# Kernel optimization log

Measured on AMD Instinct MI355X. Metric: run time of the kernel, lower is better.

The kernel has to match this reference:

```python
import jax, jax.numpy as jnp
import numpy as np

H, W, C = 384, 384, 200
HIDE, CNN_OUT, NCLS = 128, 64, 16
N = H * W
E = 1179648
EPS = 1e-5  # torch BatchNorm eps


def _bn(x, g, b, axes):
    # training-mode batch norm (biased variance), matches torch BN in train mode
    m = x.mean(axes, keepdims=True)
    v = x.var(axes, keepdims=True)
    return (x - m) * jax.lax.rsqrt(v + EPS) * g + b


def _gcn(x, w, bias, src, dst, n):
    # PyG GCNConv: add self loops, symmetric D^-1/2 (A+I) D^-1/2 normalization
    h = x @ w  # [N, out]
    loop = jnp.arange(n, dtype=src.dtype)
    s = jnp.concatenate([src, loop])
    d = jnp.concatenate([dst, loop])
    deg = jax.ops.segment_sum(jnp.ones(s.shape, x.dtype), d, num_segments=n)
    dinv = jnp.where(deg > 0, jax.lax.rsqrt(jnp.maximum(deg, 1.0)) * (deg > 0), 0.0)
    norm = dinv[s] * dinv[d]  # [E+N]
    out = jax.ops.segment_sum(h[s] * norm[:, None], d, num_segments=n)
    return out + bias


def _gnn_layer(x, bn_g, bn_b, w, b, src, dst):
    # F.normalize (row L2) -> BN1d -> GCNConv -> LeakyReLU (dropout off in eval)
    nrm = jnp.linalg.norm(x, axis=1, keepdims=True)
    x = x / jnp.maximum(nrm, 1e-12)
    x = _bn(x, bn_g, bn_b, (0,))
    return jax.nn.leaky_relu(_gcn(x, w, b, src, dst, x.shape[0]))


def setup_inputs() -> dict:
    key = jax.random.key(0)
    ks = jax.random.split(key, 16)
    p = {}
    p["x"] = jax.random.normal(ks[0], (H, W, C), jnp.float32)
    p["edge_index"] = jax.random.randint(ks[1], (2, E), 0, N, jnp.int32)
    # CNN_denoise: BN(C) -> 1x1 conv C->128 -> BN(128) -> 1x1 conv 128->128
    p["dn_bn1_g"] = jnp.ones((C,), jnp.float32); p["dn_bn1_b"] = jnp.zeros((C,), jnp.float32)
    p["dn_w1"] = jax.random.normal(ks[2], (C, HIDE), jnp.float32) * 0.05
    p["dn_b1"] = jnp.zeros((HIDE,), jnp.float32)
    p["dn_bn2_g"] = jnp.ones((HIDE,), jnp.float32); p["dn_bn2_b"] = jnp.zeros((HIDE,), jnp.float32)
    p["dn_w2"] = jax.random.normal(ks[3], (HIDE, HIDE), jnp.float32) * 0.05
    p["dn_b2"] = jnp.zeros((HIDE,), jnp.float32)
    # CNNCONV(128,64,k=5): BN(128) -> point 1x1 128->64 (no bias) -> depthwise 5x5 (bias)
    p["cnn_bn_g"] = jnp.ones((HIDE,), jnp.float32); p["cnn_bn_b"] = jnp.zeros((HIDE,), jnp.float32)
    p["cnn_pw"] = jax.random.normal(ks[4], (HIDE, CNN_OUT), jnp.float32) * 0.05
    p["cnn_dw"] = jax.random.normal(ks[5], (CNN_OUT, 1, 5, 5), jnp.float32) * 0.05
    p["cnn_db"] = jnp.zeros((CNN_OUT,), jnp.float32)
    # GCN branch: GNN(128,128), GNN(128,128), GNN(128,64)
    dims = [(HIDE, HIDE), (HIDE, HIDE), (HIDE, CNN_OUT)]
    for i, (di, do) in enumerate(dims, 1):
        p[f"g{i}_bn_g"] = jnp.ones((di,), jnp.float32)
        p[f"g{i}_bn_b"] = jnp.zeros((di,), jnp.float32)
        p[f"g{i}_w"] = jax.random.normal(ks[5 + i], (di, do), jnp.float32) * 0.05
        p[f"g{i}_b"] = jnp.zeros((do,), jnp.float32)
    p["lin_w"] = jax.random.normal(ks[9], (HIDE, NCLS), jnp.float32) * 0.05
    p["lin_b"] = jnp.zeros((NCLS,), jnp.float32)
    return p


def reference(x, edge_index,
              dn_bn1_g, dn_bn1_b, dn_w1, dn_b1, dn_bn2_g, dn_bn2_b, dn_w2, dn_b2,
              cnn_bn_g, cnn_bn_b, cnn_pw, cnn_dw, cnn_db,
              g1_bn_g, g1_bn_b, g1_w, g1_b,
              g2_bn_g, g2_bn_b, g2_w, g2_b,
              g3_bn_g, g3_bn_b, g3_w, g3_b,
              lin_w, lin_b):
    src, dst = edge_index[0], edge_index[1]
    # CNN_denoise (channel-last; 1x1 convs are matmuls)
    h = _bn(x, dn_bn1_g, dn_bn1_b, (0, 1))
    h = jax.nn.leaky_relu(h @ dn_w1 + dn_b1)
    h = _bn(h, dn_bn2_g, dn_bn2_b, (0, 1))
    clean = jax.nn.leaky_relu(h @ dn_w2 + dn_b2)       # [H,W,128]
    flat = clean.reshape(N, HIDE)
    # CNN branch: BN -> 1x1 -> LeakyReLU -> depthwise 5x5 -> LeakyReLU
    c = _bn(clean, cnn_bn_g, cnn_bn_b, (0, 1))
    c = jax.nn.leaky_relu(c @ cnn_pw)                  # [H,W,64]
    cn = c.transpose(2, 0, 1)[None]                    # [1,64,H,W]
    cn = jax.lax.conv_general_dilated(
        cn, cnn_dw, (1, 1), 'SAME', feature_group_count=CNN_OUT,
        dimension_numbers=('NCHW', 'OIHW', 'NCHW'))
    cn = jax.nn.leaky_relu(cn[0].transpose(1, 2, 0) + cnn_db)
    cnn_res = cn.reshape(N, CNN_OUT)
    # GCN branch (3 layers)
    g = _gnn_layer(flat, g1_bn_g, g1_bn_b, g1_w, g1_b, src, dst)
    g = _gnn_layer(g, g2_bn_g, g2_bn_b, g2_w, g2_b, src, dst)
    g = _gnn_layer(g, g3_bn_g, g3_bn_b, g3_w, g3_b, src, dst)
    y = jnp.concatenate([g, cnn_res], axis=-1) @ lin_w + lin_b
    return jax.nn.softmax(y, axis=-1)
```

## Files before the change

### kernel.cpp

```cpp
#include <hip/hip_runtime.h>
#include <stddef.h>

#define HH 384
#define WW 384
#define CC 200
#define NN 147456
#define EE 1179648
#define HIDE 128
#define COUT 64
#define NCLS 16
#define BN_EPS 1e-5f

#define SREP 16
#define SLOTF (512 * SREP)

using u16 = unsigned short;
typedef __attribute__((ext_vector_type(8))) short short8;
typedef __attribute__((ext_vector_type(4))) float float4v;

__device__ __forceinline__ float b2f(u16 u) {
    union { unsigned int i; float f; } v; v.i = ((unsigned int)u) << 16; return v.f;
}
__device__ __forceinline__ u16 f2b(float f) {
    union { float f; unsigned int i; } v; v.f = f;
    unsigned int x = v.i;
    unsigned int r = (x + 0x7fffu + ((x >> 16) & 1u)) >> 16;
    return (u16)r;
}
__device__ __forceinline__ float lrelu(float v) { return v > 0.f ? v : 0.01f * v; }

__global__ void sniff(const u16* __restrict__ x, int* __restrict__ flag) {
    __shared__ int cntS;
    if (threadIdx.x == 0) cntS = 0;
    __syncthreads();
    int c = 0;
    for (int i = 0; i < 8; i++) {
        u16 h = x[threadIdx.x * 8 + i];
        int hb = (h >> 8) & 0x7F;
        if (hb >= 0x3C && hb <= 0x41) c++;
    }
    atomicAdd(&cntS, c);
    __syncthreads();
    if (threadIdx.x == 0) *flag = (cntS < 1536) ? 1 : 0;
}

#define NPAR 27
struct PConv { const void* src[NPAR]; int n[NPAR]; int off[NPAR]; };

__global__ void convert_params(PConv pc, const int* __restrict__ flag,
                               u16* __restrict__ dst) {
    int b = blockIdx.x;
    int n = pc.n[b];
    const void* s = pc.src[b];
    u16* d = dst + pc.off[b];
    int isf = *flag;
    if (isf) {
        const float* sf = (const float*)s;
        for (int i = threadIdx.x; i < n; i += 256) d[i] = f2b(sf[i]);
    } else {
        const u16* sh = (const u16*)s;
        for (int i = threadIdx.x; i < n; i += 256) d[i] = sh[i];
    }
}

__global__ __launch_bounds__(256) void stats200(const void* __restrict__ X,
                                                const int* __restrict__ flag,
                                                float* __restrict__ arena) {
    __shared__ __align__(16) u16 s[128 * 200];
    int t = threadIdx.x;
    int r0 = blockIdx.x * 128;
    if (*flag) {
        const float* Xf = (const float*)X;
        for (int i = t; i < 128 * 25; i += 256) {
            int r = i / 25, kc = i - r * 25;
            const float* p = Xf + (size_t)(r0 + r) * CC + kc * 8;
            float4v a = *(const float4v*)p;
            float4v b = *(const float4v*)(p + 4);
            short8 v;
            #pragma unroll
            for (int j = 0; j < 4; j++) { v[j] = (short)f2b(a[j]); v[4 + j] = (short)f2b(b[j]); }
            *(short8*)&s[r * 200 + kc * 8] = v;
        }
    } else {
        const u16* Xh = (const u16*)X;
        for (int i = t; i < 128 * 25; i += 256) {
            int r = i / 25, kc = i - r * 25;
            *(short8*)&s[r * 200 + kc * 8] =
                *(const short8*)(Xh + (size_t)(r0 + r) * CC + kc * 8);
        }
    }
    __syncthreads();
    if (t < CC) {
        float sum = 0.f, sq = 0.f;
        for (int r = 0; r < 128; r++) {
            float v = b2f(s[r * 200 + t]);
            sum += v; sq += v * v;
        }
        float* rep = arena + (blockIdx.x & (SREP - 1)) * 512;
        atomicAdd(&rep[t], sum);
        atomicAdd(&rep[256 + t], sq);
    }
}

template<int K, int KPAD, int O>
__global__ __launch_bounds__(256) void fold_bn(
        const float* __restrict__ arena, float invN,
        const u16* __restrict__ bng, const u16* __restrict__ bnb,
        const u16* __restrict__ Wsrc, const u16* __restrict__ extrab,
        u16* __restrict__ WT, float* __restrict__ cb) {
    __shared__ float aS[KPAD], sS[KPAD];
    int t = threadIdx.x;
    if (t < KPAD) {
        float a = 0.f, sh = 0.f;
        if (t < K) {
            float sum = 0.f, sq = 0.f;
            #pragma unroll
            for (int r = 0; r < SREP; r++) {
                sum += arena[r * 512 + t];
                sq  += arena[r * 512 + 256 + t];
            }
            float m = sum * invN;
            float var = fmaxf(sq * invN - m * m, 0.f);
            a = b2f(bng[t]) * rsqrtf(var + BN_EPS);
            sh = b2f(bnb[t]) - m * a;
        }
        aS[t] = a; sS[t] = sh;
    }
    __syncthreads();
    int g = t >> 6, l = t & 63;
    int o = blockIdx.x * 4 + g;
    if (o < O) {
        float c = 0.f;
        #pragma unroll
        for (int k = l; k < KPAD; k += 64) {
            float w = (k < K) ? b2f(Wsrc[k * O + o]) : 0.f;
            c += sS[k] * w;
            WT[o * KPAD + k] = f2b(aS[k] * w);
        }
        #pragma unroll
        for (int s = 32; s >= 1; s >>= 1) c += __shfl_down(c, s);
        if (l == 0) cb[o] = c + (extrab ? b2f(extrab[o]) : 0.f);
    }
}

template<int KT, int KSRC, int O, bool LEAKY, bool SCALE, int STATS, bool DUAL>
__global__ __launch_bounds__(256) void gemm_mfma(
        const void* __restrict__ Ap, const u16* __restrict__ WT,
        const float* __restrict__ cb, const float* __restrict__ s1,
        const float* __restrict__ s2, const int* __restrict__ f32p,
        u16* __restrict__ out, float* __restrict__ stA,
        float* __restrict__ stB, float* __restrict__ invn,
        u16* __restrict__ out2) {
    constexpr int KPAD = KT * 32;
    constexpr int LDA = KPAD + 8;
    constexpr int CHR = KPAD / 8;
    constexpr int CHD = KSRC / 8;
    constexpr int NCT = O / 16;
    constexpr int CPW = NCT / 4;
    __shared__ __align__(16) u16 As[64 * LDA];
    __shared__ float rS[4][64];
    __shared__ float invS[64];
    __shared__ float sS1[64], sS2[64];
    int tid = threadIdx.x;
    int row0 = blockIdx.x * 64;

    int isf = f32p ? *f32p : 0;
    if (isf) {
        const float* A = (const float*)Ap;
        for (int i = tid; i < 64 * CHR; i += 256) {
            int r = i / CHR, kc = i - r * CHR;
            short8 v = {0, 0, 0, 0, 0, 0, 0, 0};
            if (kc < CHD) {
                const float* p = A + (size_t)(row0 + r) * KSRC + kc * 8;
                float4v a = *(const float4v*)p;
                float4v b = *(const float4v*)(p + 4);
                #pragma unroll
                for (int j = 0; j < 4; j++) { v[j] = (short)f2b(a[j]); v[4 + j] = (short)f2b(b[j]); }
            }
            *(short8*)&As[r * LDA + kc * 8] = v;
        }
    } else {
        const u16* A = (const u16*)Ap;
        for (int i = tid; i < 64 * CHR; i += 256) {
            int r = i / CHR, kc = i - r * CHR;
            short8 v = {0, 0, 0, 0, 0, 0, 0, 0};
            if (kc < CHD)
                v = *(const short8*)(A + (size_t)(row0 + r) * KSRC + kc * 8);
            *(short8*)&As[r * LDA + kc * 8] = v;
        }
    }
    if (SCALE && tid < 64) { sS1[tid] = s1[row0 + tid]; sS2[tid] = s2[row0 + tid]; }
    __syncthreads();

    int w = tid >> 6, lane = tid & 63, m = lane & 15, q = lane >> 4;
    float4v acc[4][CPW];
    #pragma unroll
    for (int mf = 0; mf < 4; mf++)
        #pragma unroll
        for (int cp = 0; cp < CPW; cp++)
            acc[mf][cp] = (float4v){0.f, 0.f, 0.f, 0.f};

    const u16* Abp = &As[m * LDA + q * 8];
    const u16* Bbp = WT + (size_t)((w * CPW) * 16 + m) * KPAD + q * 8;

    #pragma unroll
    for (int kt = 0; kt < KT; kt++) {
        short8 af[4];
        #pragma unroll
        for (int mf = 0; mf < 4; mf++)
            af[mf] = *(const short8*)(Abp + mf * 16 * LDA + kt * 32);
        #pragma unroll
        for (int cp = 0; cp < CPW; cp++) {
            short8 bf = *(const short8*)(Bbp + (size_t)cp * 16 * KPAD + kt * 32);
            #pragma unroll
            for (int mf = 0; mf < 4; mf++)
                acc[mf][cp] = __builtin_amdgcn_mfma_f32_16x16x32_bf16(
                    af[mf], bf, acc[mf][cp], 0, 0, 0);
        }
    }

    float rp[4][4] = {};
    #pragma unroll
    for (int cp = 0; cp < CPW; cp++) {
        int ct = w * CPW + cp;
        int col = ct * 16 + m;
        float cbv = cb[col];
        #pragma unroll
        for (int mf = 0; mf < 4; mf++) {
            #pragma unroll
            for (int r = 0; r < 4; r++) {
                int rl = mf * 16 + q * 4 + r;
                float x = acc[mf][cp][r];
                if constexpr (DUAL) {
                    if (ct < 8) {
                        x = (x * sS1[rl] + cbv) * sS2[rl];
                        out[(size_t)(row0 + rl) * 128 + col] = f2b(x);
                    } else {
                        x = lrelu(x + cbv);
                        out2[(size_t)(row0 + rl) * 64 + (col - 128)] = f2b(x);
                    }
                } else {
                    if constexpr (SCALE) x = (x * sS1[rl] + cbv) * sS2[rl];
                    else                 x += cbv;
                    if constexpr (LEAKY) x = lrelu(x);
                    out[(size_t)(row0 + rl) * O + col] = f2b(x);
                }
                acc[mf][cp][r] = x;
                if constexpr (STATS == 2) rp[mf][r] += x * x;
            }
        }
    }

    if constexpr (STATS == 2) {
        #pragma unroll
        for (int mf = 0; mf < 4; mf++) {
            #pragma unroll
            for (int r = 0; r < 4; r++) {
                float v = rp[mf][r];
                v += __shfl_xor(v, 1); v += __shfl_xor(v, 2);
                v += __shfl_xor(v, 4); v += __shfl_xor(v, 8);
                if (m == 0) rS[w][mf * 16 + q * 4 + r] = v;
            }
        }
        __syncthreads();
        if (tid < 64) {
            float ss = rS[0][tid] + rS[1][tid] + rS[2][tid] + rS[3][tid];
            float inv = 1.0f / fmaxf(sqrtf(ss), 1e-12f);
            invS[tid] = inv;
            invn[row0 + tid] = inv;
        }
        __syncthreads();
    }

    if constexpr (STATS >= 1) {
        float* stAr = stA + (blockIdx.x & (SREP - 1)) * 512;
        float* stBr = (STATS == 2) ? stB + (blockIdx.x & (SREP - 1)) * 512 : nullptr;
        #pragma unroll
        for (int cp = 0; cp < CPW; cp++) {
            int col = (w * CPW + cp) * 16 + m;
            float cs = 0.f, cq = 0.f, ns = 0.f, nq = 0.f;
            #pragma unroll
            for (int mf = 0; mf < 4; mf++) {
                #pragma unroll
                for (int r = 0; r < 4; r++) {
                    float x = acc[mf][cp][r];
                    cs += x; cq += x * x;
                    if constexpr (STATS == 2) {
                        float nv = x * invS[mf * 16 + q * 4 + r];
                        ns += nv; nq += nv * nv;
                    }
                }
            }
            cs += __shfl_xor(cs, 16); cs += __shfl_xor(cs, 32);
            cq += __shfl_xor(cq, 16); cq += __shfl_xor(cq, 32);
            if constexpr (STATS == 2) {
                ns += __shfl_xor(ns, 16); ns += __shfl_xor(ns, 32);
                nq += __shfl_xor(nq, 16); nq += __shfl_xor(nq, 32);
            }
            if (q == 0) {
                atomicAdd(&stAr[col], cs);
                atomicAdd(&stAr[256 + col], cq);
                if constexpr (STATS == 2) {
                    atomicAdd(&stBr[col], ns);
                    atomicAdd(&stBr[256 + col], nq);
                }
            }
        }
    }
}

__global__ void hist(const int* __restrict__ dst, int* __restrict__ cnt) {
    int e = blockIdx.x * 256 + threadIdx.x;
    unsigned d = (unsigned)dst[e];
    if (d < (unsigned)NN) atomicAdd(&cnt[d], 1);
}
__global__ void mkdinv(const int* __restrict__ cnt, float* __restrict__ dinv) {
    int i = blockIdx.x * 256 + threadIdx.x;
    int c = cnt[i]; if (c < 0) c = 0;
    dinv[i] = rsqrtf((float)c + 1.0f);
}
__global__ void scan_part(const int* __restrict__ cnt, int* __restrict__ bsum) {
    int b = blockIdx.x, t = threadIdx.x;
    int base = b * 1024 + t * 4;
    int s = cnt[base] + cnt[base + 1] + cnt[base + 2] + cnt[base + 3];
    #pragma unroll
    for (int o = 32; o >= 1; o >>= 1) s += __shfl_down(s, o);
    __shared__ int ws4[4];
    if ((t & 63) == 0) ws4[t >> 6] = s;
    __syncthreads();
    if (t == 0) bsum[b] = ws4[0] + ws4[1] + ws4[2] + ws4[3];
}
__global__ void scan_top(const int* __restrict__ bsum, int* __restrict__ boff) {
    if (threadIdx.x == 0) {
        int a = 0;
        for (int i = 0; i < 144; i++) { boff[i] = a; a += bsum[i]; }
    }
}
__global__ void scan_write(const int* __restrict__ cnt, const int* __restrict__ boff,
                           int* __restrict__ offv) {
    int b = blockIdx.x, t = threadIdx.x;
    int base = b * 1024 + t * 4;
    int v0 = cnt[base], v1 = cnt[base + 1], v2 = cnt[base + 2], v3 = cnt[base + 3];
    int ts = v0 + v1 + v2 + v3;
    __shared__ int sc[256];
    sc[t] = ts;
    __syncthreads();
    for (int o = 1; o < 256; o <<= 1) {
        int x = (t >= o) ? sc[t - o] : 0;
        __syncthreads();
        sc[t] += x;
        __syncthreads();
    }
    int excl = boff[b] + sc[t] - ts;
    offv[base] = excl;
    offv[base + 1] = excl + v0;
    offv[base + 2] = excl + v0 + v1;
    offv[base + 3] = excl + v0 + v1 + v2;
    if (b == 143 && t == 255) offv[NN] = excl + ts;
}
__global__ void scatter(const int* __restrict__ src, const int* __restrict__ dst,
                        int* __restrict__ cursor, const int* __restrict__ offv,
                        int* __restrict__ csr) {
    int e = blockIdx.x * 256 + threadIdx.x;
    unsigned d = (unsigned)dst[e];
    if (d >= (unsigned)NN) return;
    int p = atomicAdd(&cursor[d], 1);
    unsigned idx = (unsigned)(offv[d] + p);
    if (idx < (unsigned)EE) csr[idx] = src[e];
}

template<int O, int STATS, int GRP>
__global__ __launch_bounds__(256) void aggregate(
        const u16* __restrict__ h2, const int* __restrict__ offv,
        const int* __restrict__ csr, const float* __restrict__ dinv,
        const u16* __restrict__ gb, u16* __restrict__ outp,
        float* __restrict__ stA, float* __restrict__ invn) {
    constexpr int CH = O / 8;
    constexpr int NPB = 256 / CH;
    __shared__ float colS[O], colQ[O];
    int t = threadIdx.x;
    if (STATS && t < O) { colS[t] = 0.f; colQ[t] = 0.f; }
    int local = t / CH, c = t % CH;
    size_t cof = (size_t)c * 8;
    const u16* hb = h2 + cof;
    short8 gv = *(const short8*)(gb + cof);
    float sreg[8] = {0.f, 0.f, 0.f, 0.f, 0.f, 0.f, 0.f, 0.f};
    float qreg[8] = {0.f, 0.f, 0.f, 0.f, 0.f, 0.f, 0.f, 0.f};

    #pragma unroll
    for (int g = 0; g < GRP; g++) {
        int d = blockIdx.x * (NPB * GRP) + g * NPB + local;
        float acc[8];
        short8 selfv = *(const short8*)(hb + (size_t)d * O);
        #pragma unroll
        for (int j = 0; j < 8; j++) acc[j] = b2f((u16)selfv[j]);
        int e0 = offv[d], e1 = offv[d + 1];
        if (e0 < 0) e0 = 0;
        if (e1 > EE) e1 = EE;
        int k = e0;
        int nq = (e1 - e0) >> 2;
        unsigned ia = 0, ib = 0, ic2 = 0, id2 = 0;
        if (nq > 0) {
            ia  = (unsigned)csr[k];     ib  = (unsigned)csr[k + 1];
            ic2 = (unsigned)csr[k + 2]; id2 = (unsigned)csr[k + 3];
        }
        for (int qi = 0; qi < nq; qi++) {
            short8 va = *(const short8*)(hb + (size_t)ia * O);
            short8 vb = *(const short8*)(hb + (size_t)ib * O);
            short8 vc = *(const short8*)(hb + (size_t)ic2 * O);
            short8 vd = *(const short8*)(hb + (size_t)id2 * O);
            k += 4;
            if (qi + 1 < nq) {
                ia  = (unsigned)csr[k];     ib  = (unsigned)csr[k + 1];
                ic2 = (unsigned)csr[k + 2]; id2 = (unsigned)csr[k + 3];
            }
            #pragma unroll
            for (int j = 0; j < 8; j++)
                acc[j] += (b2f((u16)va[j]) + b2f((u16)vb[j])) +
                          (b2f((u16)vc[j]) + b2f((u16)vd[j]));
        }
        for (; k < e1; k++) {
            unsigned s = (unsigned)csr[k];
            short8 va = *(const short8*)(hb + (size_t)s * O);
            #pragma unroll
            for (int j = 0; j < 8; j++) acc[j] += b2f((u16)va[j]);
        }
        float dd = dinv[d];
        float outv[8];
        short8 res;
        #pragma unroll
        for (int j = 0; j < 8; j++) {
            outv[j] = lrelu(dd * acc[j] + b2f((u16)gv[j]));
            res[j] = (short)f2b(outv[j]);
        }
        *(short8*)(outp + (size_t)d * O + cof) = res;

        if constexpr (STATS) {
            float ss = 0.f;
            #pragma unroll
            for (int j = 0; j < 8; j++) ss += outv[j] * outv[j];
            ss += __shfl_xor(ss, 1); ss += __shfl_xor(ss, 2);
            ss += __shfl_xor(ss, 4); ss += __shfl_xor(ss, 8);
            float inv = 1.0f / fmaxf(sqrtf(ss), 1e-12f);
            if (c == 0) invn[d] = inv;
            #pragma unroll
            for (int j = 0; j < 8; j++) {
                float nv = outv[j] * inv;
                sreg[j] += nv; qreg[j] += nv * nv;
            }
        }
    }

    if constexpr (STATS) {
        __syncthreads();
        #pragma unroll
        for (int j = 0; j < 8; j++) {
            float s = sreg[j];
            s += __shfl_xor(s, 16); s += __shfl_xor(s, 32);
            float qq = qreg[j];
            qq += __shfl_xor(qq, 16); qq += __shfl_xor(qq, 32);
            if ((t & 63) < 16) {
                atomicAdd(&colS[c * 8 + j], s);
                atomicAdd(&colQ[c * 8 + j], qq);
            }
        }
        __syncthreads();
        if (t < O) {
            float* rep = stA + (blockIdx.x & (SREP - 1)) * 512;
            atomicAdd(&rep[t], colS[t]);
            atomicAdd(&rep[256 + t], colQ[t]);
        }
    }
}

__global__ __launch_bounds__(256) void final_fused(
        const u16* __restrict__ g3, const u16* __restrict__ cpre,
        const u16* __restrict__ dwW, const u16* __restrict__ db,
        const u16* __restrict__ lw, const u16* __restrict__ lb,
        const int* __restrict__ flag, void* __restrict__ outp) {
    __shared__ __align__(16) u16 tile[400 * 72];
    __shared__ __align__(16) u16 wT[25 * 64];
    __shared__ __align__(16) u16 wL[2048];
    __shared__ float bDW[64];
    __shared__ float bL[16];
    int t = threadIdx.x;
    int tx = blockIdx.x % 24, ty = blockIdx.x / 24;
    int x0 = tx * 16 - 2, y0 = ty * 16 - 2;
    for (int i = t; i < 1600; i += 256) {
        int f = i / 25, tap = i - f * 25;
        wT[tap * 64 + f] = dwW[i];
    }
    for (int i = t; i < 2048; i += 256) wL[i] = lw[i];
    if (t < 64) bDW[t] = b2f(db[t]);
    if (t < 16) bL[t] = b2f(lb[t]);
    for (int u = t; u < 3200; u += 256) {
        int pix = u >> 3, c8 = u & 7;
        int gy = y0 + pix / 20, gx = x0 + pix % 20;
        short8 v = {0, 0, 0, 0, 0, 0, 0, 0};
        if (gy >= 0 && gy < HH && gx >= 0 && gx < WW)
            v = *(const short8*)(cpre + ((size_t)(gy * WW + gx)) * 64 + c8 * 8);
        *(short8*)&tile[pix * 72 + c8 * 8] = v;
    }
    __syncthreads();

    int px = t & 15, py = t >> 4;
    int node = (ty * 16 + py) * WW + tx * 16 + px;
    float y[16];
    #pragma unroll
    for (int o = 0; o < 16; o++) y[o] = bL[o];

    const u16* g3p = g3 + (size_t)node * 64;
    for (int c8 = 0; c8 < 8; c8++) {
        short8 gvv = *(const short8*)(g3p + c8 * 8);
        #pragma unroll
        for (int j = 0; j < 8; j++) {
            float g = b2f((u16)gvv[j]);
            const short8 w0 = *(const short8*)&wL[(c8 * 8 + j) * 16];
            const short8 w1 = *(const short8*)&wL[(c8 * 8 + j) * 16 + 8];
            #pragma unroll
            for (int o = 0; o < 8; o++) {
                y[o]     += g * b2f((u16)w0[o]);
                y[o + 8] += g * b2f((u16)w1[o]);
            }
        }
    }
    for (int c8 = 0; c8 < 8; c8++) {
        float acc[8] = {0.f, 0.f, 0.f, 0.f, 0.f, 0.f, 0.f, 0.f};
        #pragma unroll
        for (int dy = 0; dy < 5; dy++) {
            int rbase = ((py + dy) * 20 + px) * 72 + c8 * 8;
            #pragma unroll
            for (int dx = 0; dx < 5; dx++) {
                short8 v  = *(const short8*)&tile[rbase + dx * 72];
                short8 wv = *(const short8*)&wT[(dy * 5 + dx) * 64 + c8 * 8];
                #pragma unroll
                for (int j = 0; j < 8; j++)
                    acc[j] += b2f((u16)v[j]) * b2f((u16)wv[j]);
            }
        }
        #pragma unroll
        for (int j = 0; j < 8; j++) {
            float cv = lrelu(acc[j] + bDW[c8 * 8 + j]);
            int f = 64 + c8 * 8 + j;
            const short8 w0 = *(const short8*)&wL[f * 16];
            const short8 w1 = *(const short8*)&wL[f * 16 + 8];
            #pragma unroll
            for (int o = 0; o < 8; o++) {
                y[o]     += cv * b2f((u16)w0[o]);
                y[o + 8] += cv * b2f((u16)w1[o]);
            }
        }
    }
    float mx = y[0];
    #pragma unroll
    for (int o = 1; o < 16; o++) mx = fmaxf(mx, y[o]);
    float sum = 0.f;
    #pragma unroll
    for (int o = 0; o < 16; o++) { y[o] = __expf(y[o] - mx); sum += y[o]; }
    float inv = 1.0f / fmaxf(sum, 1e-30f);
    if (*flag) {
        float* of = (float*)outp;
        #pragma unroll
        for (int o = 0; o < 16; o++) of[(size_t)node * 16 + o] = y[o] * inv;
    } else {
        u16* oh = (u16*)outp;
        #pragma unroll
        for (int o = 0; o < 16; o++) oh[(size_t)node * 16 + o] = f2b(y[o] * inv);
    }
}

extern "C" void kernel_launch(void* const* d_in, const int* in_sizes, int n_in,
                              void* d_out, int out_size, void* d_ws, size_t ws_size,
                              hipStream_t stream) {
    const void* X   = d_in[0];
    const int* EIDX = (const int*)d_in[1];
    const int* esrc = EIDX;
    const int* edst = EIDX + EE;

    char* ws = (char*)d_ws;
    size_t off = 0;
    auto alloc = [&](size_t sz) -> char* {
        size_t szr = (sz + 255) & ~(size_t)255;
        char* p;
        if (off + szr <= ws_size) { p = ws + off; off += szr; }
        else { p = ws; }
        return p;
    };

    int*   dflag   = (int*)alloc(256);
    static const int pidx[NPAR] = {2,3,4,5,6,7,8,9,10,11,12,13,14,
                                   15,16,17,18,19,20,21,22,23,24,25,26,27,28};
    static const int pn[NPAR]   = {200,200,25600,128,128,128,16384,128,
                                   128,128,8192,1600,64,
                                   128,128,16384,128,
                                   128,128,16384,128,
                                   128,128,8192,64,
                                   2048,16};
    u16* parena = (u16*)alloc(100352 * 2);
    PConv pc;
    {
        int po = 0;
        for (int i = 0; i < NPAR; i++) {
            pc.src[i] = d_in[pidx[i]];
            pc.n[i] = pn[i];
            pc.off[i] = po;
            po += (pn[i] + 15) & ~15;
        }
    }
    const u16* DN1G = parena + pc.off[0];
    const u16* DN1B = parena + pc.off[1];
    const u16* DNW1 = parena + pc.off[2];
    const u16* DNB1 = parena + pc.off[3];
    const u16* DN2G = parena + pc.off[4];
    const u16* DN2B = parena + pc.off[5];
    const u16* DNW2 = parena + pc.off[6];
    const u16* DNB2 = parena + pc.off[7];
    const u16* CBNG = parena + pc.off[8];
    const u16* CBNB = parena + pc.off[9];
    const u16* CPW  = parena + pc.off[10];
    const u16* CDW  = parena + pc.off[11];
    const u16* CDB  = parena + pc.off[12];
    const u16* G1G  = parena + pc.off[13];
    const u16* G1B  = parena + pc.off[14];
    const u16* G1W  = parena + pc.off[15];
    const u16* G1BI = parena + pc.off[16];
    const u16* G2G  = parena + pc.off[17];
    const u16* G2B  = parena + pc.off[18];
    const u16* G2W  = parena + pc.off[19];
    const u16* G2BI = parena + pc.off[20];
    const u16* G3G  = parena + pc.off[21];
    const u16* G3B  = parena + pc.off[22];
    const u16* G3W  = parena + pc.off[23];
    const u16* G3BI = parena + pc.off[24];
    const u16* LINW = parena + pc.off[25];
    const u16* LINB = parena + pc.off[26];

    int*   cnt     = (int*)alloc((size_t)NN * 4);
    int*   cursor  = (int*)alloc((size_t)NN * 4);
    float* arena   = (float*)alloc((size_t)6 * SLOTF * 4);
    int*   offv    = (int*)alloc((size_t)(NN + 1) * 4);
    int*   bsum    = (int*)alloc(144 * 4);
    int*   boff    = (int*)alloc(144 * 4);
    float* dinvp   = (float*)alloc((size_t)NN * 4);
    float* invnorm = (float*)alloc((size_t)NN * 4);
    u16*   W1T     = (u16*)alloc(128 * 224 * 2);
    u16*   W2T     = (u16*)alloc(128 * 128 * 2);
    u16*   WgT     = (u16*)alloc(192 * 128 * 2);
    float* cb1     = (float*)alloc(128 * 4);
    float* cb2     = (float*)alloc(128 * 4);
    float* cbg     = (float*)alloc(192 * 4);
    int*   csr     = (int*)alloc((size_t)EE * 4);
    u16*   cbuf    = (u16*)alloc((size_t)NN * 64 * 2);
    u16*   big1    = (u16*)alloc((size_t)NN * 128 * 2);
    u16*   big2    = (u16*)alloc((size_t)NN * 128 * 2);

    const float invN = 1.0f / (float)NN;
    size_t zsz = (size_t)((char*)(arena + 6 * SLOTF) - (char*)cnt);
    size_t zcap = ((char*)cnt >= ws && (size_t)((char*)cnt - ws) < ws_size)
                      ? ws_size - (size_t)((char*)cnt - ws) : 0;
    if (zsz > zcap) zsz = zcap;
    hipMemsetAsync(cnt, 0, zsz, stream);

    sniff<<<1, 256, 0, stream>>>((const u16*)X, dflag);
    convert_params<<<NPAR, 256, 0, stream>>>(pc, dflag, parena);

    hist<<<EE / 256, 256, 0, stream>>>(edst, cnt);
    mkdinv<<<NN / 256, 256, 0, stream>>>(cnt, dinvp);
    scan_part<<<144, 256, 0, stream>>>(cnt, bsum);
    scan_top<<<1, 64, 0, stream>>>(bsum, boff);
    scan_write<<<144, 256, 0, stream>>>(cnt, boff, offv);
    scatter<<<EE / 256, 256, 0, stream>>>(esrc, edst, cursor, offv, csr);

    stats200<<<1152, 256, 0, stream>>>(X, dflag, arena + 0 * SLOTF);
    fold_bn<200, 224, 128><<<32, 256, 0, stream>>>(arena + 0 * SLOTF, invN, DN1G, DN1B, DNW1, DNB1, W1T, cb1);
    gemm_mfma<7, 200, 128, true, false, 1, false><<<NN / 64, 256, 0, stream>>>(
        X, W1T, cb1, nullptr, nullptr, dflag, big1, arena + 1 * SLOTF, nullptr, nullptr, nullptr);
    fold_bn<128, 128, 128><<<32, 256, 0, stream>>>(arena + 1 * SLOTF, invN, DN2G, DN2B, DNW2, DNB2, W2T, cb2);
    gemm_mfma<4, 128, 128, true, false, 2, false><<<NN / 64, 256, 0, stream>>>(
        big1, W2T, cb2, nullptr, nullptr, nullptr, big2, arena + 2 * SLOTF, arena + 3 * SLOTF, invnorm, nullptr);

    fold_bn<128, 128, 128><<<32, 256, 0, stream>>>(arena + 3 * SLOTF, invN, G1G, G1B, G1W, nullptr, WgT, cbg);
    fold_bn<128, 128, 64><<<16, 256, 0, stream>>>(arena + 2 * SLOTF, invN, CBNG, CBNB, CPW, nullptr,
                                                  WgT + 128 * 128, cbg + 128);
    gemm_mfma<4, 128, 192, false, true, 0, true><<<NN / 64, 256, 0, stream>>>(
        big2, WgT, cbg, invnorm, dinvp, nullptr, big1, nullptr, nullptr, nullptr, cbuf);
    aggregate<128, 1, 4><<<NN / 64, 256, 0, stream>>>(
        big1, offv, csr, dinvp, G1BI, big2, arena + 4 * SLOTF, invnorm);

    fold_bn<128, 128, 128><<<32, 256, 0, stream>>>(arena + 4 * SLOTF, invN, G2G, G2B, G2W, nullptr, WgT, cbg);
    gemm_mfma<4, 128, 128, false, true, 0, false><<<NN / 64, 256, 0, stream>>>(
        big2, WgT, cbg, invnorm, dinvp, nullptr, big1, nullptr, nullptr, nullptr, nullptr);
    aggregate<128, 1, 4><<<NN / 64, 256, 0, stream>>>(
        big1, offv, csr, dinvp, G2BI, big2, arena + 5 * SLOTF, invnorm);

    fold_bn<128, 128, 64><<<16, 256, 0, stream>>>(arena + 5 * SLOTF, invN, G3G, G3B, G3W, nullptr, WgT, cbg);
    gemm_mfma<4, 128, 64, false, true, 0, false><<<NN / 64, 256, 0, stream>>>(
        big2, WgT, cbg, invnorm, dinvp, nullptr, big1, nullptr, nullptr, nullptr, nullptr);
    aggregate<64, 0, 1><<<NN / 32, 256, 0, stream>>>(
        big1, offv, csr, dinvp, G3BI, big2, nullptr, nullptr);

    final_fused<<<576, 256, 0, stream>>>(big2, cbuf, CDW, CDB, LINW, LINB, dflag, d_out);

    (void)in_sizes; (void)n_in; (void)out_size;
}
```

Before: 770.0 us.

## Sort nodes by degree for load-balanced GCN aggregation and unroll gather by 8

Builds a degree-bucketed permutation of nodes (histogram, scan, scatter) and makes each aggregate kernel process nodes in that order, so lanes in a wavefront handle similar-degree nodes and divergence drops. The neighbor gather loop is also restructured to issue 8 independent row loads per iteration with 4/2/1 tails, raising memory-level parallelism. The cost is three extra small kernels, an extra indirection through perm, and loss of spatial locality in output writes and self-row reads.

```diff
diff --git a/kernel.cpp b/kernel.cpp
--- a/kernel.cpp
+++ b/kernel.cpp
@@ -13,6 +13,7 @@
 
 #define SREP 16
 #define SLOTF (512 * SREP)
+#define DBINS 64
 
 using u16 = unsigned short;
 typedef __attribute__((ext_vector_type(8))) short short8;
@@ -369,12 +370,46 @@
     if (idx < (unsigned)EE) csr[idx] = src[e];
 }
 
+__global__ void deg_hist(const int* __restrict__ cnt, int* __restrict__ dbin) {
+    __shared__ int h[DBINS];
+    int t = threadIdx.x;
+    if (t < DBINS) h[t] = 0;
+    __syncthreads();
+    int i = blockIdx.x * 256 + t;
+    int dg = cnt[i]; if (dg < 0) dg = 0; if (dg > DBINS - 1) dg = DBINS - 1;
+    atomicAdd(&h[dg], 1);
+    __syncthreads();
+    if (t < DBINS) atomicAdd(&dbin[t], h[t]);
+}
+__global__ void deg_scan(const int* __restrict__ dbin, int* __restrict__ dbase) {
+    if (threadIdx.x == 0) {
+        int a = 0;
+        for (int b = DBINS - 1; b >= 0; b--) { dbase[b] = a; a += dbin[b]; }
+    }
+}
+__global__ void deg_scatter(const int* __restrict__ cnt, int* __restrict__ dbase,
+                            int* __restrict__ perm) {
+    __shared__ int h[DBINS], base[DBINS];
+    int t = threadIdx.x;
+    if (t < DBINS) h[t] = 0;
+    __syncthreads();
+    int i = blockIdx.x * 256 + t;
+    int dg = cnt[i]; if (dg < 0) dg = 0; if (dg > DBINS - 1) dg = DBINS - 1;
+    atomicAdd(&h[dg], 1);
+    __syncthreads();
+    if (t < DBINS) { base[t] = atomicAdd(&dbase[t], h[t]); h[t] = 0; }
+    __syncthreads();
+    int lp = atomicAdd(&h[dg], 1);
+    perm[base[dg] + lp] = i;
+}
+
 template<int O, int STATS, int GRP>
 __global__ __launch_bounds__(256) void aggregate(
         const u16* __restrict__ h2, const int* __restrict__ offv,
         const int* __restrict__ csr, const float* __restrict__ dinv,
         const u16* __restrict__ gb, u16* __restrict__ outp,
-        float* __restrict__ stA, float* __restrict__ invn) {
+        float* __restrict__ stA, float* __restrict__ invn,
+        const int* __restrict__ perm) {
     constexpr int CH = O / 8;
     constexpr int NPB = 256 / CH;
     __shared__ float colS[O], colQ[O];
@@ -389,7 +424,8 @@
 
     #pragma unroll
     for (int g = 0; g < GRP; g++) {
-        int d = blockIdx.x * (NPB * GRP) + g * NPB + local;
+        int pos = blockIdx.x * (NPB * GRP) + g * NPB + local;
+        int d = perm[pos];
         float acc[8];
         short8 selfv = *(const short8*)(hb + (size_t)d * O);
         #pragma unroll
@@ -398,32 +434,53 @@
         if (e0 < 0) e0 = 0;
         if (e1 > EE) e1 = EE;
         int k = e0;
-        int nq = (e1 - e0) >> 2;
-        unsigned ia = 0, ib = 0, ic2 = 0, id2 = 0;
-        if (nq > 0) {
-            ia  = (unsigned)csr[k];     ib  = (unsigned)csr[k + 1];
-            ic2 = (unsigned)csr[k + 2]; id2 = (unsigned)csr[k + 3];
-        }
-        for (int qi = 0; qi < nq; qi++) {
-            short8 va = *(const short8*)(hb + (size_t)ia * O);
-            short8 vb = *(const short8*)(hb + (size_t)ib * O);
-            short8 vc = *(const short8*)(hb + (size_t)ic2 * O);
-            short8 vd = *(const short8*)(hb + (size_t)id2 * O);
+        for (; k + 8 <= e1; k += 8) {
+            unsigned i0 = (unsigned)csr[k],     i1 = (unsigned)csr[k + 1];
+            unsigned i2 = (unsigned)csr[k + 2], i3 = (unsigned)csr[k + 3];
+            unsigned i4 = (unsigned)csr[k + 4], i5 = (unsigned)csr[k + 5];
+            unsigned i6 = (unsigned)csr[k + 6], i7 = (unsigned)csr[k + 7];
+            short8 v0 = *(const short8*)(hb + (size_t)i0 * O);
+            short8 v1 = *(const short8*)(hb + (size_t)i1 * O);
+            short8 v2 = *(const short8*)(hb + (size_t)i2 * O);
+            short8 v3 = *(const short8*)(hb + (size_t)i3 * O);
+            short8 v4 = *(const short8*)(hb + (size_t)i4 * O);
+            short8 v5 = *(const short8*)(hb + (size_t)i5 * O);
+            short8 v6 = *(const short8*)(hb + (size_t)i6 * O);
+            short8 v7 = *(const short8*)(hb + (size_t)i7 * O);
+            #pragma unroll
+            for (int j = 0; j < 8; j++)
+                acc[j] += ((b2f((u16)v0[j]) + b2f((u16)v1[j])) +
+                           (b2f((u16)v2[j]) + b2f((u16)v3[j]))) +
+                          ((b2f((u16)v4[j]) + b2f((u16)v5[j])) +
+                           (b2f((u16)v6[j]) + b2f((u16)v7[j])));
+        }
+        if (k + 4 <= e1) {
+            unsigned i0 = (unsigned)csr[k],     i1 = (unsigned)csr[k + 1];
+            unsigned i2 = (unsigned)csr[k + 2], i3 = (unsigned)csr[k + 3];
+            short8 v0 = *(const short8*)(hb + (size_t)i0 * O);
+            short8 v1 = *(const short8*)(hb + (size_t)i1 * O);
+            short8 v2 = *(const short8*)(hb + (size_t)i2 * O);
+            short8 v3 = *(const short8*)(hb + (size_t)i3 * O);
+            #pragma unroll
+            for (int j = 0; j < 8; j++)
+                acc[j] += (b2f((u16)v0[j]) + b2f((u16)v1[j])) +
+                          (b2f((u16)v2[j]) + b2f((u16)v3[j]));
             k += 4;
-            if (qi + 1 < nq) {
-                ia  = (unsigned)csr[k];     ib  = (unsigned)csr[k + 1];
-                ic2 = (unsigned)csr[k + 2]; id2 = (unsigned)csr[k + 3];
-            }
+        }
+        if (k + 2 <= e1) {
+            unsigned i0 = (unsigned)csr[k], i1 = (unsigned)csr[k + 1];
+            short8 v0 = *(const short8*)(hb + (size_t)i0 * O);
+            short8 v1 = *(const short8*)(hb + (size_t)i1 * O);
             #pragma unroll
             for (int j = 0; j < 8; j++)
-                acc[j] += (b2f((u16)va[j]) + b2f((u16)vb[j])) +
-                          (b2f((u16)vc[j]) + b2f((u16)vd[j]));
-        }
-        for (; k < e1; k++) {
-            unsigned s = (unsigned)csr[k];
-            short8 va = *(const short8*)(hb + (size_t)s * O);
-            #pragma unroll
-            for (int j = 0; j < 8; j++) acc[j] += b2f((u16)va[j]);
+                acc[j] += b2f((u16)v0[j]) + b2f((u16)v1[j]);
+            k += 2;
+        }
+        if (k < e1) {
+            unsigned i0 = (unsigned)csr[k];
+            short8 v0 = *(const short8*)(hb + (size_t)i0 * O);
+            #pragma unroll
+            for (int j = 0; j < 8; j++) acc[j] += b2f((u16)v0[j]);
         }
         float dd = dinv[d];
         float outv[8];
@@ -638,9 +695,12 @@
     int*   cnt     = (int*)alloc((size_t)NN * 4);
     int*   cursor  = (int*)alloc((size_t)NN * 4);
     float* arena   = (float*)alloc((size_t)6 * SLOTF * 4);
+    int*   dbin    = (int*)alloc(DBINS * 4);
     int*   offv    = (int*)alloc((size_t)(NN + 1) * 4);
     int*   bsum    = (int*)alloc(144 * 4);
     int*   boff    = (int*)alloc(144 * 4);
+    int*   dbase   = (int*)alloc(DBINS * 4);
+    int*   perm    = (int*)alloc((size_t)NN * 4);
     float* dinvp   = (float*)alloc((size_t)NN * 4);
     float* invnorm = (float*)alloc((size_t)NN * 4);
     u16*   W1T     = (u16*)alloc(128 * 224 * 2);
@@ -655,7 +715,7 @@
     u16*   big2    = (u16*)alloc((size_t)NN * 128 * 2);
 
     const float invN = 1.0f / (float)NN;
-    size_t zsz = (size_t)((char*)(arena + 6 * SLOTF) - (char*)cnt);
+    size_t zsz = (size_t)((char*)dbin + 256 - (char*)cnt);
     size_t zcap = ((char*)cnt >= ws && (size_t)((char*)cnt - ws) < ws_size)
                       ? ws_size - (size_t)((char*)cnt - ws) : 0;
     if (zsz > zcap) zsz = zcap;
@@ -666,6 +726,9 @@
 
     hist<<<EE / 256, 256, 0, stream>>>(edst, cnt);
     mkdinv<<<NN / 256, 256, 0, stream>>>(cnt, dinvp);
+    deg_hist<<<NN / 256, 256, 0, stream>>>(cnt, dbin);
+    deg_scan<<<1, 64, 0, stream>>>(dbin, dbase);
+    deg_scatter<<<NN / 256, 256, 0, stream>>>(cnt, dbase, perm);
     scan_part<<<144, 256, 0, stream>>>(cnt, bsum);
     scan_top<<<1, 64, 0, stream>>>(bsum, boff);
     scan_write<<<144, 256, 0, stream>>>(cnt, boff, offv);
@@ -685,19 +748,19 @@
     gemm_mfma<4, 128, 192, false, true, 0, true><<<NN / 64, 256, 0, stream>>>(
         big2, WgT, cbg, invnorm, dinvp, nullptr, big1, nullptr, nullptr, nullptr, cbuf);
     aggregate<128, 1, 4><<<NN / 64, 256, 0, stream>>>(
-        big1, offv, csr, dinvp, G1BI, big2, arena + 4 * SLOTF, invnorm);
+        big1, offv, csr, dinvp, G1BI, big2, arena + 4 * SLOTF, invnorm, perm);
 
     fold_bn<128, 128, 128><<<32, 256, 0, stream>>>(arena + 4 * SLOTF, invN, G2G, G2B, G2W, nullptr, WgT, cbg);
     gemm_mfma<4, 128, 128, false, true, 0, false><<<NN / 64, 256, 0, stream>>>(
         big2, WgT, cbg, invnorm, dinvp, nullptr, big1, nullptr, nullptr, nullptr, nullptr);
     aggregate<128, 1, 4><<<NN / 64, 256, 0, stream>>>(
-        big1, offv, csr, dinvp, G2BI, big2, arena + 5 * SLOTF, invnorm);
+        big1, offv, csr, dinvp, G2BI, big2, arena + 5 * SLOTF, invnorm, perm);
 
     fold_bn<128, 128, 64><<<16, 256, 0, stream>>>(arena + 5 * SLOTF, invN, G3G, G3B, G3W, nullptr, WgT, cbg);
     gemm_mfma<4, 128, 64, false, true, 0, false><<<NN / 64, 256, 0, stream>>>(
         big2, WgT, cbg, invnorm, dinvp, nullptr, big1, nullptr, nullptr, nullptr, nullptr);
     aggregate<64, 0, 1><<<NN / 32, 256, 0, stream>>>(
-        big1, offv, csr, dinvp, G3BI, big2, nullptr, nullptr);
+        big1, offv, csr, dinvp, G3BI, big2, nullptr, nullptr, perm);
 
     final_fused<<<576, 256, 0, stream>>>(big2, cbuf, CDW, CDB, LINW, LINB, dflag, d_out);
 
```

After: 798.7 us. 1.04x slower.
